# Kernel optimization log

Measured on AMD Instinct MI355X. Metric: run time of the kernel, lower is better.

The kernel has to match this reference:

```python
import jax, jax.numpy as jnp
import numpy as np
from jax import lax

NUM_ENT = 100000
NUM_REL = 100          # init_rel has 2*NUM_REL rows (forward + inverse relations)
DIM = 200              # init_dim = gcn_dim = embed_dim
E = 1000000
B = 1024
K_H, K_W = 10, 20      # embed_dim == k_h * k_w
NUM_FILT = 200
KER = 7
FLAT_H = 2 * K_H - KER + 1   # 14
FLAT_W = K_W - KER + 1       # 14
FLAT_SZ = FLAT_H * FLAT_W * NUM_FILT  # 39200


def _bn1d(x, g, b, eps=1e-5):
    # training-mode BatchNorm1d (biased variance, matching torch)
    m = x.mean(0)
    v = x.var(0)
    return (x - m) * lax.rsqrt(v + eps) * g + b


def _bn2d(x, g, b, eps=1e-5):
    m = x.mean((0, 2, 3), keepdims=True)
    v = x.var((0, 2, 3), keepdims=True)
    return (x - m) * lax.rsqrt(v + eps) * g[None, :, None, None] + b[None, :, None, None]


def _compgcn_layer(x, r, src, dst, etype, enorm,
                   w_in, w_out, w_loop, w_rel, loop_rel, bias, gamma, beta):
    # CompGCNCov with opn='mult': comp(h_src, rel) = h_src * rel
    half = etype.shape[0] // 2
    comp = x[src] * r[etype]                                   # [E, din] edge gather + compose
    msg = jnp.concatenate([comp[:half] @ w_in,                 # first half: original edges
                           comp[half:] @ w_out], axis=0)       # second half: inverse edges
    msg = msg * enorm[:, None]
    agg = jax.ops.segment_sum(msg, dst, num_segments=NUM_ENT)  # scatter-sum to dst nodes
    loop = (x * loop_rel) @ w_loop                             # self-loop composition
    h = (agg + loop) * (1.0 / 3.0) + bias
    h = _bn1d(h, gamma, beta)
    return jnp.tanh(h), r @ w_rel


def setup_inputs() -> dict:
    key = jax.random.key(0)
    ks = jax.random.split(key, 40)
    f32 = jnp.float32
    s = 1.0 / np.sqrt(DIM)
    inp = {
        "init_embed": jax.random.normal(ks[0], (NUM_ENT, DIM), f32) * s,
        "init_rel":   jax.random.normal(ks[1], (2 * NUM_REL, DIM), f32) * s,
        "edge_norm":  jax.random.uniform(ks[2], (E,), f32),
    }
    names = ["w_in", "w_out", "w_loop", "w_rel"]
    for layer in (1, 2):
        for i, n in enumerate(names):
            inp[f"{n}{layer}"] = jax.random.normal(ks[3 + 6 * layer + i], (DIM, DIM), f32) * s
        inp[f"loop_rel{layer}"] = jax.random.normal(jax.random.fold_in(key, layer), (1, DIM), f32) * s
        inp[f"b{layer}"] = jnp.zeros((DIM,), f32)
        inp[f"g{layer}"] = jnp.ones((DIM,), f32)
        inp[f"be{layer}"] = jnp.zeros((DIM,), f32)
    inp["conv_w"] = jax.random.normal(ks[20], (NUM_FILT, 1, KER, KER), f32) * (1.0 / KER)
    inp["conv_b"] = jnp.zeros((NUM_FILT,), f32)
    inp["fc_w"] = jax.random.normal(ks[21], (DIM, FLAT_SZ), f32) * (1.0 / np.sqrt(FLAT_SZ))
    inp["fc_b"] = jnp.zeros((DIM,), f32)
    for n, c in (("bn0", 1), ("bn1", NUM_FILT), ("bn2", DIM)):
        inp[f"{n}_g"] = jnp.ones((c,), f32)
        inp[f"{n}_b"] = jnp.zeros((c,), f32)
    inp["subj"] = jax.random.randint(ks[22], (B,), 0, NUM_ENT)
    inp["rel_idx"] = jax.random.randint(ks[23], (B,), 0, 2 * NUM_REL)
    inp["obj"] = jax.random.randint(ks[24], (B,), 0, NUM_ENT)
    inp["src"] = jax.random.randint(ks[25], (E,), 0, NUM_ENT)
    inp["dst"] = jax.random.randint(ks[26], (E,), 0, NUM_ENT)
    inp["edge_type"] = jnp.concatenate([
        jax.random.randint(ks[27], (E // 2,), 0, NUM_REL),          # in-edges
        jax.random.randint(ks[28], (E // 2,), NUM_REL, 2 * NUM_REL)])  # inverse edges
    return inp


def reference(init_embed, init_rel, edge_norm,
              w_in1, w_out1, w_loop1, w_rel1, loop_rel1, b1, g1, be1,
              w_in2, w_out2, w_loop2, w_rel2, loop_rel2, b2, g2, be2,
              conv_w, conv_b, fc_w, fc_b,
              bn0_g, bn0_b, bn1_g, bn1_b, bn2_g, bn2_b,
              subj, rel_idx, obj, src, dst, edge_type):
    # --- GCN encoder: 2 CompGCN layers ---
    x, r = _compgcn_layer(init_embed, init_rel, src, dst, edge_type, edge_norm,
                          w_in1, w_out1, w_loop1, w_rel1, loop_rel1, b1, g1, be1)
    x, r = _compgcn_layer(x, r, src, dst, edge_type, edge_norm,
                          w_in2, w_out2, w_loop2, w_rel2, loop_rel2, b2, g2, be2)
    sub_emb, rel_emb, obj_emb = x[subj], r[rel_idx], x[obj]   # [B, DIM] each
    # --- ConvE scoring head ---
    stk = jnp.concatenate([sub_emb[:, None, :], rel_emb[:, None, :]], 1)
    stk = stk.reshape(B, 1, 2 * K_H, K_W)                     # [B,1,20,20]
    h = _bn2d(stk, bn0_g, bn0_b)
    h = lax.conv_general_dilated(h, conv_w, (1, 1), 'VALID',
                                 dimension_numbers=('NCHW', 'OIHW', 'NCHW'))
    h = h + conv_b[None, :, None, None]                       # [B,NUM_FILT,14,14]
    h = jnp.maximum(_bn2d(h, bn1_g, bn1_b), 0.0)
    h = h.reshape(B, FLAT_SZ) @ fc_w.T + fc_b                 # [B, DIM]
    h = jnp.maximum(_bn1d(h, bn2_g, bn2_b), 0.0)
    return jax.nn.sigmoid(h @ obj_emb.T)                      # [B, B]
```

## Files before the change

kernel.cpp:

```cpp
#include <hip/hip_runtime.h>

#define DIM 200
#define NENT 100000
#define NEDGE 1000000
#define EHALF 500000
#define NB 1024
#define NFILT 200
#define FLATSZ 39200

#define NDF ((size_t)NENT * DIM)
#define REGF ((size_t)20100000)
#define WPLANE (208 * 224)

typedef float floatx4 __attribute__((ext_vector_type(4)));
typedef short bf16x8 __attribute__((ext_vector_type(8)));
typedef short bf16x4 __attribute__((ext_vector_type(4)));
typedef _Float16 halfx8 __attribute__((ext_vector_type(8)));
typedef _Float16 halfx4 __attribute__((ext_vector_type(4)));

__device__ __forceinline__ void gAtomicAdd(float* p, float v) { unsafeAtomicAdd(p, v); }
__device__ __forceinline__ void gAtomicAdd(double* p, double v) { unsafeAtomicAdd(p, v); }

__device__ __forceinline__ short f2bf(float f) {
    union { float f; unsigned u; } v; v.f = f;
    unsigned r = v.u + 0x7fffu + ((v.u >> 16) & 1u);
    return (short)(r >> 16);
}
__device__ __forceinline__ float bf2f(short s) {
    union { float f; unsigned u; } v; v.u = ((unsigned)(unsigned short)s) << 16;
    return v.f;
}
__device__ __forceinline__ short f2bf_t(float f) {
    union { float f; unsigned u; } v; v.f = f;
    return (short)(v.u >> 16);
}
__device__ __forceinline__ void split8t(const floatx4& lo4, const floatx4& hi4,
                                        bf16x8& h, bf16x8& l) {
#pragma unroll
    for (int e = 0; e < 4; ++e) {
        short hh = f2bf_t(lo4[e]); h[e] = hh; l[e] = f2bf_t(lo4[e] - bf2f(hh));
        short hh2 = f2bf_t(hi4[e]); h[e + 4] = hh2; l[e + 4] = f2bf_t(hi4[e] - bf2f(hh2));
    }
}
__device__ __forceinline__ void split4r(const float4& v, bf16x4& h, bf16x4& l) {
    float a0 = v.x, a1 = v.y, a2 = v.z, a3 = v.w;
    short h0 = f2bf(a0), h1 = f2bf(a1), h2 = f2bf(a2), h3 = f2bf(a3);
    h[0] = h0; h[1] = h1; h[2] = h2; h[3] = h3;
    l[0] = f2bf(a0 - bf2f(h0)); l[1] = f2bf(a1 - bf2f(h1));
    l[2] = f2bf(a2 - bf2f(h2)); l[3] = f2bf(a3 - bf2f(h3));
}

__global__ __launch_bounds__(256) void edge_hist(
    const int* __restrict__ dst, int* __restrict__ hist)
{
    int stride = gridDim.x * blockDim.x;
    for (int e = blockIdx.x * 256 + threadIdx.x; e < NEDGE; e += stride)
        atomicAdd(&hist[dst[e]], 1);
}

__global__ __launch_bounds__(256) void scan1(
    const int* __restrict__ hist, int* __restrict__ incl, int* __restrict__ bsum)
{
    __shared__ int sm[256];
    int i = blockIdx.x * 256 + threadIdx.x;
    int t = threadIdx.x;
    sm[t] = (i < NENT) ? hist[i] : 0;
    __syncthreads();
    for (int off = 1; off < 256; off <<= 1) {
        int v = (t >= off) ? sm[t - off] : 0;
        __syncthreads();
        sm[t] += v;
        __syncthreads();
    }
    if (i < NENT) incl[i] = sm[t];
    if (t == 255) bsum[blockIdx.x] = sm[255];
}

__global__ __launch_bounds__(512) void scan2(int* bsum, int nb)
{
    __shared__ int sm[512];
    int t = threadIdx.x;
    int v = (t < nb) ? bsum[t] : 0;
    sm[t] = v;
    __syncthreads();
    for (int off = 1; off < 512; off <<= 1) {
        int u = (t >= off) ? sm[t - off] : 0;
        __syncthreads();
        sm[t] += u;
        __syncthreads();
    }
    if (t < nb) bsum[t] = sm[t] - v;
}

__global__ __launch_bounds__(256) void scan3(
    const int* __restrict__ hist, int* __restrict__ offs,
    const int* __restrict__ bsum, int* __restrict__ cursor)
{
    int i = blockIdx.x * 256 + threadIdx.x;
    if (i < NENT) {
        int excl = offs[i] - hist[i] + bsum[blockIdx.x];
        offs[i] = excl;
        cursor[i] = excl;
    }
    if (i == 0) offs[NENT] = NEDGE;
}

__global__ __launch_bounds__(256) void edge_fill(
    const int* __restrict__ src, const int* __restrict__ dst,
    const int* __restrict__ etype, const float* __restrict__ enorm,
    int* __restrict__ cursor, int4* __restrict__ recs)
{
    int stride = gridDim.x * blockDim.x;
    for (int e = blockIdx.x * 256 + threadIdx.x; e < NEDGE; e += stride) {
        int pos = atomicAdd(&cursor[dst[e]], 1);
        recs[pos] = make_int4(src[e], etype[e] | ((e >= EHALF) ? 0x10000 : 0),
                              __float_as_int(enorm[e]), 0);
    }
}

__global__ __launch_bounds__(256) void build_map(
    const int* __restrict__ subj, const int* __restrict__ obj, int* __restrict__ map)
{
    int i = blockIdx.x * 256 + threadIdx.x;
    if (i < NB) map[subj[i]] = i;
    else if (i < 2 * NB) map[obj[i - NB]] = i;
}

__global__ __launch_bounds__(256) void to_f16(
    const float* __restrict__ X, _Float16* __restrict__ Y, long n4)
{
    long stride = (long)gridDim.x * blockDim.x;
    for (long i = (long)blockIdx.x * blockDim.x + threadIdx.x; i < n4; i += stride) {
        float4 v = ((const float4*)X)[i];
        halfx4 h;
        h[0] = (_Float16)v.x; h[1] = (_Float16)v.y;
        h[2] = (_Float16)v.z; h[3] = (_Float16)v.w;
        ((halfx4*)Y)[i] = h;
    }
}

__global__ __launch_bounds__(256) void gather_nodes(
    const _Float16* __restrict__ x16, const float* __restrict__ r,
    const int* __restrict__ offs, const int4* __restrict__ recs,
    short* __restrict__ aggI, short* __restrict__ aggO)
{
    int node = blockIdx.x * 4 + (threadIdx.x >> 6);
    int lane = threadIdx.x & 63;
    if (node >= NENT) return;
    int beg = offs[node], end = offs[node + 1];
    bool act = lane < 50;
    int lane_c = min(lane, 49);
    const float4* rb = (const float4*)r;
    float4 aI = make_float4(0.f, 0.f, 0.f, 0.f);
    float4 aO = make_float4(0.f, 0.f, 0.f, 0.f);

    auto ld_x = [&](int s) -> float4 {
        halfx4 v = *(const halfx4*)&x16[(size_t)s * 200 + lane_c * 4];
        return make_float4((float)v[0], (float)v[1], (float)v[2], (float)v[3]);
    };

    if (beg < end) {
        int i1 = min(beg + 1, end - 1);
        int4 rcA = recs[beg];
        int4 rcB = recs[i1];
        float4 xvA = ld_x(rcA.x);
        float4 rvA = rb[(size_t)(rcA.y & 0xffff) * 50 + lane_c];
        for (int i = beg; i < end; ++i) {
            int i2 = min(i + 2, end - 1);
            int4 rcC = recs[i2];
            float4 xvB = ld_x(rcB.x);
            float4 rvB = rb[(size_t)(rcB.y & 0xffff) * 50 + lane_c];
            float w = __int_as_float(rcA.z);
            float wI = (rcA.y & 0x10000) ? 0.f : w;
            float wO = w - wI;
            float px = xvA.x * rvA.x, py = xvA.y * rvA.y,
                  pz = xvA.z * rvA.z, pw = xvA.w * rvA.w;
            aI.x += px * wI; aI.y += py * wI; aI.z += pz * wI; aI.w += pw * wI;
            aO.x += px * wO; aO.y += py * wO; aO.z += pz * wO; aO.w += pw * wO;
            rcA = rcB; rcB = rcC; xvA = xvB; rvA = rvB;
        }
    }
    if (act) {
        bf16x4 hI, lI, hO, lO;
        split4r(aI, hI, lI);
        split4r(aO, hO, lO);
        size_t base = (size_t)node * 400 + lane * 4;
        *(bf16x4*)&aggI[base] = hI;
        *(bf16x4*)&aggI[base + 200] = lI;
        *(bf16x4*)&aggO[base] = hO;
        *(bf16x4*)&aggO[base + 200] = lO;
    }
}

__global__ __launch_bounds__(256) void pack_w3(
    const float* __restrict__ w0, const float* __restrict__ w1,
    const float* __restrict__ w2, const float* __restrict__ lrel,
    short* __restrict__ Wp)
{
    int i = blockIdx.x * 256 + threadIdx.x;
    if (i >= 3 * WPLANE) return;
    int seg = i / WPLANE, rem = i % WPLANE;
    int n = rem / 224, k = rem % 224;
    const float* W = (seg == 0) ? w0 : (seg == 1) ? w1 : w2;
    float v = (n < 200 && k < 200) ? W[k * 200 + n] : 0.f;
    if (seg == 2 && n < 200 && k < 200) v *= lrel[k];
    short hi = f2bf(v);
    Wp[i] = hi;
    Wp[i + 3 * WPLANE] = f2bf(v - bf2f(hi));
}

__global__ __launch_bounds__(256) void pack_fcw(
    const float* __restrict__ W, _Float16* __restrict__ Wt)
{
    long i = (long)blockIdx.x * 256 + threadIdx.x;
    if (i >= (long)208 * FLATSZ) return;
    int n = (int)(i / FLATSZ);
    Wt[i] = (n < 200) ? (_Float16)W[i] : (_Float16)0.f;
}

template<int NF0, int NF, int A2MODE>
__device__ __forceinline__ void gemm_body(
    const short* __restrict__ A0s, const short* __restrict__ A1s,
    const float* __restrict__ A2f, const _Float16* __restrict__ A2h,
    const short* __restrict__ WpH, const short* __restrict__ WpL,
    float* C, const float* __restrict__ bias, const int* __restrict__ map,
    float alpha, int M, double* __restrict__ s1, double* __restrict__ s2,
    short* BsH, short* BsL, float* fsum, float* fsq)
{
    int t = threadIdx.x;
    int lane = t & 63, wave = t >> 6;
    int col16 = lane & 15, quad = lane >> 4;
    int row_base = blockIdx.x * 128 + wave * 32;
    if (t < 112) { fsum[t] = 0.f; fsq[t] = 0.f; }
    floatx4 acc[NF][2];
#pragma unroll
    for (int nf = 0; nf < NF; ++nf) { acc[nf][0] = (floatx4)0.f; acc[nf][1] = (floatx4)0.f; }
    int r0 = row_base + col16, r1 = row_base + 16 + col16;
    int r0c = min(r0, M - 1), r1c = min(r1, M - 1);
    size_t b0 = (size_t)r0c * 400, b1 = (size_t)r1c * 400;
    const int rows4 = NF * 16 * 4;

    bf16x8 sh[2], sl[2];
    bf16x8 cah0 = (bf16x8)0, cal0 = (bf16x8)0,
           cah1 = (bf16x8)0, cal1 = (bf16x8)0;
    bf16x8 nah0 = (bf16x8)0, nal0 = (bf16x8)0,
           nah1 = (bf16x8)0, nal1 = (bf16x8)0;

    auto stage_ld = [&](int kc) {
        int seg = kc / 7, c = kc - seg * 7, k0 = c * 32;
        const short* WH = WpH + seg * WPLANE + k0;
        const short* WL = WpL + seg * WPLANE + k0;
#pragma unroll
        for (int s = 0; s < 2; ++s) {
            int i = t + s * 256;
            if (i < rows4) {
                int nl = i >> 2, part = i & 3;
                int n = NF0 * 16 + nl;
                sh[s] = *(const bf16x8*)&WH[n * 224 + part * 8];
                sl[s] = *(const bf16x8*)&WL[n * 224 + part * 8];
            }
        }
    };
    auto stage_st = [&](short* BH, short* BL) {
#pragma unroll
        for (int s = 0; s < 2; ++s) {
            int i = t + s * 256;
            if (i < rows4) {
                int nl = i >> 2, part = i & 3;
                *(bf16x8*)&BH[nl * 40 + part * 8] = sh[s];
                *(bf16x8*)&BL[nl * 40 + part * 8] = sl[s];
            }
        }
    };
    auto loadA = [&](int kc, bf16x8& h0, bf16x8& l0, bf16x8& h1, bf16x8& l1) {
        int seg = kc / 7, c = kc - seg * 7;
        int koff = c * 32 + quad * 8;
        if (koff < 200) {
            if (seg < 2) {
                const short* A = seg ? A1s : A0s;
                h0 = *(const bf16x8*)&A[b0 + koff];
                l0 = *(const bf16x8*)&A[b0 + 200 + koff];
                h1 = *(const bf16x8*)&A[b1 + koff];
                l1 = *(const bf16x8*)&A[b1 + 200 + koff];
            } else {
                size_t o0 = (size_t)r0c * 200 + koff, o1 = (size_t)r1c * 200 + koff;
                floatx4 x0, x1v, y0, y1v;
                if (A2MODE == 0) {
                    x0 = *(const floatx4*)&A2f[o0];
                    x1v = *(const floatx4*)&A2f[o0 + 4];
                    y0 = *(const floatx4*)&A2f[o1];
                    y1v = *(const floatx4*)&A2f[o1 + 4];
                } else {
                    halfx8 v0 = *(const halfx8*)&A2h[o0];
                    halfx8 v1 = *(const halfx8*)&A2h[o1];
#pragma unroll
                    for (int e = 0; e < 4; ++e) {
                        x0[e] = (float)v0[e]; x1v[e] = (float)v0[e + 4];
                        y0[e] = (float)v1[e]; y1v[e] = (float)v1[e + 4];
                    }
                }
                split8t(x0, x1v, h0, l0);
                split8t(y0, y1v, h1, l1);
            }
        } else {
            h0 = (bf16x8)0; l0 = (bf16x8)0; h1 = (bf16x8)0; l1 = (bf16x8)0;
        }
    };

    stage_ld(0);
    loadA(0, cah0, cal0, cah1, cal1);
    stage_st(BsH, BsL);
    __syncthreads();

    for (int kc = 0; kc < 21; ++kc) {
        int cur = kc & 1;
        const short* BH = BsH + cur * 4480;
        const short* BL = BsL + cur * 4480;
        if (kc < 20) {
            stage_ld(kc + 1);
            loadA(kc + 1, nah0, nal0, nah1, nal1);
        }
        __builtin_amdgcn_s_setprio(1);
#pragma unroll
        for (int nf = 0; nf < NF; ++nf) {
            bf16x8 bh = *(const bf16x8*)&BH[(nf * 16 + col16) * 40 + quad * 8];
            bf16x8 bl = *(const bf16x8*)&BL[(nf * 16 + col16) * 40 + quad * 8];
            acc[nf][0] = __builtin_amdgcn_mfma_f32_16x16x32_bf16(cah0, bh, acc[nf][0], 0, 0, 0);
            acc[nf][0] = __builtin_amdgcn_mfma_f32_16x16x32_bf16(cah0, bl, acc[nf][0], 0, 0, 0);
            acc[nf][0] = __builtin_amdgcn_mfma_f32_16x16x32_bf16(cal0, bh, acc[nf][0], 0, 0, 0);
            acc[nf][1] = __builtin_amdgcn_mfma_f32_16x16x32_bf16(cah1, bh, acc[nf][1], 0, 0, 0);
            acc[nf][1] = __builtin_amdgcn_mfma_f32_16x16x32_bf16(cah1, bl, acc[nf][1], 0, 0, 0);
            acc[nf][1] = __builtin_amdgcn_mfma_f32_16x16x32_bf16(cal1, bh, acc[nf][1], 0, 0, 0);
        }
        __builtin_amdgcn_s_setprio(0);
        if (kc < 20) {
            short* BHn = BsH + (cur ^ 1) * 4480;
            short* BLn = BsL + (cur ^ 1) * 4480;
            stage_st(BHn, BLn);
        }
        __syncthreads();
        cah0 = nah0; cal0 = nal0; cah1 = nah1; cal1 = nal1;
    }

    int slot[2][4];
    if (map) {
#pragma unroll
        for (int h = 0; h < 2; ++h)
#pragma unroll
            for (int j = 0; j < 4; ++j) {
                int rr = row_base + h * 16 + quad * 4 + j;
                slot[h][j] = (rr < M) ? map[rr] : -1;
            }
    }
#pragma unroll
    for (int nf = 0; nf < NF; ++nf) {
        int lc = nf * 16 + col16;
        int colg = NF0 * 16 + lc;
        if (colg >= 200) continue;
        float bv = bias[colg];
        float ls = 0.f, lq = 0.f;
#pragma unroll
        for (int h = 0; h < 2; ++h) {
            int rbase = row_base + h * 16 + quad * 4;
#pragma unroll
            for (int j = 0; j < 4; ++j) {
                int rr = rbase + j;
                if (rr < M) {
                    float v = acc[nf][h][j] * alpha + bv;
                    ls += v; lq += v * v;
                    if (!map) {
                        C[(size_t)rr * 200 + colg] = v;
                    } else {
                        int s = slot[h][j];
                        if (s >= 0) C[(size_t)s * 200 + colg] = v;
                    }
                }
            }
        }
        ls += __shfl_down(ls, 32); ls += __shfl_down(ls, 16);
        lq += __shfl_down(lq, 32); lq += __shfl_down(lq, 16);
        if (quad == 0) {
            atomicAdd(&fsum[lc], ls);
            atomicAdd(&fsq[lc], lq);
        }
    }
    __syncthreads();
    if (t < NF * 16) {
        int colg = NF0 * 16 + t;
        if (colg < 200) {
            gAtomicAdd(&s1[colg], (double)fsum[t]);
            gAtomicAdd(&s2[colg], (double)fsq[t]);
        }
    }
}

template<int A2MODE>
__global__ __launch_bounds__(256) void gemm_mfma(
    const short* A0s, const short* A1s,
    const float* A2f, const _Float16* A2h,
    const short* __restrict__ WpH, const short* __restrict__ WpL,
    float* C, const float* __restrict__ bias, const int* __restrict__ map,
    float alpha, int M, double* __restrict__ s1, double* __restrict__ s2)
{
    __shared__ short BsH[2][112 * 40];
    __shared__ short BsL[2][112 * 40];
    __shared__ float fsum[112];
    __shared__ float fsq[112];
    if (blockIdx.y == 0)
        gemm_body<0, 7, A2MODE>(A0s, A1s, A2f, A2h, WpH, WpL, C, bias, map,
                                alpha, M, s1, s2, &BsH[0][0], &BsL[0][0], fsum, fsq);
    else
        gemm_body<7, 6, A2MODE>(A0s, A1s, A2f, A2h, WpH, WpL, C, bias, map,
                                alpha, M, s1, s2, &BsH[0][0], &BsL[0][0], fsum, fsq);
}

template<int NF0, int NF>
__device__ __forceinline__ void fc_gemm_body(
    const _Float16* __restrict__ Ph, const _Float16* __restrict__ Wt,
    float* __restrict__ part, int ky, _Float16* Bs)
{
    int t = threadIdx.x;
    int lane = t & 63, wave = t >> 6;
    int col16 = lane & 15, quad = lane >> 4;
    int row_base = blockIdx.x * 128 + wave * 32;
    int c0 = ky * 25;
    floatx4 acc[NF][2];
#pragma unroll
    for (int nf = 0; nf < NF; ++nf) { acc[nf][0] = (floatx4)0.f; acc[nf][1] = (floatx4)0.f; }
    int r0 = row_base + col16, r1 = row_base + 16 + col16;
    const int rows4 = NF * 16 * 4;

    for (int c = c0; c < c0 + 25; ++c) {
        int k0 = c * 32;
        for (int i = t; i < rows4; i += 256) {
            int nl = i >> 2, part_i = i & 3;
            int n = NF0 * 16 + nl;
            *(halfx8*)&Bs[nl * 40 + part_i * 8] =
                *(const halfx8*)&Wt[(size_t)n * FLATSZ + k0 + part_i * 8];
        }
        __syncthreads();
        int koff = k0 + quad * 8;
        halfx8 a0 = *(const halfx8*)&Ph[(size_t)r0 * FLATSZ + koff];
        halfx8 a1 = *(const halfx8*)&Ph[(size_t)r1 * FLATSZ + koff];
#pragma unroll
        for (int nf = 0; nf < NF; ++nf) {
            halfx8 b = *(const halfx8*)&Bs[(nf * 16 + col16) * 40 + quad * 8];
            acc[nf][0] = __builtin_amdgcn_mfma_f32_16x16x32_f16(a0, b, acc[nf][0], 0, 0, 0);
            acc[nf][1] = __builtin_amdgcn_mfma_f32_16x16x32_f16(a1, b, acc[nf][1], 0, 0, 0);
        }
        __syncthreads();
    }
    float* out = part + (size_t)ky * (NB * 200);
#pragma unroll
    for (int nf = 0; nf < NF; ++nf) {
        int colg = NF0 * 16 + nf * 16 + col16;
        if (colg >= 200) continue;
#pragma unroll
        for (int h = 0; h < 2; ++h) {
            int rbase = row_base + h * 16 + quad * 4;
#pragma unroll
            for (int j = 0; j < 4; ++j)
                out[(size_t)(rbase + j) * 200 + colg] = acc[nf][h][j];
        }
    }
}

__global__ __launch_bounds__(256) void fc_gemm(
    const _Float16* __restrict__ Ph, const _Float16* __restrict__ Wt,
    float* __restrict__ part)
{
    __shared__ _Float16 Bs[112 * 40];
    int ky = blockIdx.y >> 1;
    if ((blockIdx.y & 1) == 0)
        fc_gemm_body<0, 7>(Ph, Wt, part, ky, Bs);
    else
        fc_gemm_body<7, 6>(Ph, Wt, part, ky, Bs);
}

__global__ __launch_bounds__(256) void fc_reduce(
    const float* __restrict__ part, const float* __restrict__ bias,
    float* __restrict__ hfc)
{
    int i = blockIdx.x * 256 + threadIdx.x;
    float acc = bias[i % 200];
#pragma unroll
    for (int y = 0; y < 49; ++y) acc += part[(size_t)y * (NB * 200) + i];
    hfc[i] = acc;
}

__global__ __launch_bounds__(256) void colstats(
    const float* __restrict__ X, int M, int rpb,
    double* __restrict__ s1, double* __restrict__ s2)
{
    int c = threadIdx.x;
    if (c >= 200) return;
    int r0 = blockIdx.x * rpb;
    int r1 = min(r0 + rpb, M);
    float sum = 0.f, sq = 0.f;
    for (int rr = r0; rr < r1; ++rr) {
        float v = X[(size_t)rr * 200 + c];
        sum += v; sq += v * v;
    }
    gAtomicAdd(&s1[c], (double)sum);
    gAtomicAdd(&s2[c], (double)sq);
}

__global__ void finalize_stats(const double* __restrict__ s1, const double* __restrict__ s2,
                               const float* __restrict__ g, const float* __restrict__ bb,
                               float* __restrict__ sc, float* __restrict__ sh,
                               int ncols, double count)
{
    int c = threadIdx.x;
    if (c >= ncols) return;
    double m = s1[c] / count;
    double v = s2[c] / count - m * m;
    double scd = (double)g[c] / sqrt(v + 1e-5);
    sc[c] = (float)scd;
    sh[c] = (float)((double)bb[c] - m * scd);
}

__global__ __launch_bounds__(256) void bn_tanh_f16(
    const float* __restrict__ X, const float* __restrict__ sc,
    const float* __restrict__ sh, _Float16* __restrict__ Y, long n4)
{
    long stride = (long)gridDim.x * blockDim.x;
    for (long i = (long)blockIdx.x * blockDim.x + threadIdx.x; i < n4; i += stride) {
        int c4 = (int)(i % 50) * 4;
        float4 v = ((const float4*)X)[i];
        halfx4 h;
        h[0] = (_Float16)tanhf(v.x * sc[c4 + 0] + sh[c4 + 0]);
        h[1] = (_Float16)tanhf(v.y * sc[c4 + 1] + sh[c4 + 1]);
        h[2] = (_Float16)tanhf(v.z * sc[c4 + 2] + sh[c4 + 2]);
        h[3] = (_Float16)tanhf(v.w * sc[c4 + 3] + sh[c4 + 3]);
        ((halfx4*)Y)[i] = h;
    }
}

__global__ __launch_bounds__(256) void bn_act_200(
    float* __restrict__ X, const float* __restrict__ sc, const float* __restrict__ sh,
    long n4, int act)
{
    long stride = (long)gridDim.x * blockDim.x;
    for (long i = (long)blockIdx.x * blockDim.x + threadIdx.x; i < n4; i += stride) {
        int c4 = (int)(i % 50) * 4;
        float4 v = ((const float4*)X)[i];
        float a0 = v.x * sc[c4 + 0] + sh[c4 + 0];
        float a1 = v.y * sc[c4 + 1] + sh[c4 + 1];
        float a2 = v.z * sc[c4 + 2] + sh[c4 + 2];
        float a3 = v.w * sc[c4 + 3] + sh[c4 + 3];
        if (act == 0) { a0 = tanhf(a0); a1 = tanhf(a1); a2 = tanhf(a2); a3 = tanhf(a3); }
        else { a0 = fmaxf(a0, 0.f); a1 = fmaxf(a1, 0.f); a2 = fmaxf(a2, 0.f); a3 = fmaxf(a3, 0.f); }
        ((float4*)X)[i] = make_float4(a0, a1, a2, a3);
    }
}

__global__ __launch_bounds__(256) void rel_mm(
    const float* __restrict__ R, const float* __restrict__ W, float* __restrict__ O)
{
    int idx = blockIdx.x * blockDim.x + threadIdx.x;
    if (idx >= 200 * 200) return;
    int row = idx / 200, col = idx - row * 200;
    float acc = 0.f;
    for (int k = 0; k < 200; ++k) acc = fmaf(R[row * 200 + k], W[k * 200 + col], acc);
    O[idx] = acc;
}

__global__ __launch_bounds__(256) void build_stk(
    const float* __restrict__ x2c, const float* __restrict__ r2,
    const int* __restrict__ subj, const int* __restrict__ ridx,
    const int* __restrict__ map,
    float* __restrict__ stk, double* __restrict__ s1, double* __restrict__ s2)
{
    __shared__ float wsum[4], wsq[4];
    int b = blockIdx.x, t = threadIdx.x;
    const float* se = x2c + (size_t)map[subj[b]] * DIM;
    const float* re = r2 + (size_t)ridx[b] * DIM;
    float sum = 0.f, sq = 0.f;
    for (int i = t; i < 400; i += 256) {
        float v = (i < 200) ? se[i] : re[i - 200];
        stk[(size_t)b * 400 + i] = v;
        sum += v; sq += v * v;
    }
    for (int off = 32; off > 0; off >>= 1) {
        sum += __shfl_down(sum, off);
        sq  += __shfl_down(sq, off);
    }
    if ((t & 63) == 0) { wsum[t >> 6] = sum; wsq[t >> 6] = sq; }
    __syncthreads();
    if (t == 0) {
        float S = wsum[0] + wsum[1] + wsum[2] + wsum[3];
        float Q = wsq[0] + wsq[1] + wsq[2] + wsq[3];
        gAtomicAdd(&s1[0], (double)S);
        gAtomicAdd(&s2[0], (double)Q);
    }
}

__global__ __launch_bounds__(256) void conv_fwd(
    const float* __restrict__ stk, const float* __restrict__ conv_w,
    const float* __restrict__ conv_b, const float* __restrict__ sc0,
    const float* __restrict__ sh0, _Float16* __restrict__ Ph,
    double* __restrict__ s1, double* __restrict__ s2)
{
    __shared__ float img[400];
    __shared__ float wsm[9800];
    __shared__ float bsm[200];
    __shared__ float fsum[200];
    __shared__ float fsq[200];
    int b = blockIdx.x, t = threadIdx.x;
    float scale0 = sc0[0], shift0 = sh0[0];
    if (t < 200) { fsum[t] = 0.f; fsq[t] = 0.f; bsm[t] = conv_b[t]; }
    for (int i = t; i < 400; i += 256) img[i] = stk[(size_t)b * 400 + i] * scale0 + shift0;
    for (int i = t; i < 9800; i += 256) wsm[i] = conv_w[i];
    __syncthreads();
    for (int fy = t; fy < 2800; fy += 256) {
        int f = fy / 14, y = fy - (fy / 14) * 14;
        const float* wf = &wsm[f * 49];
        float acc[14];
        float bias = bsm[f];
#pragma unroll
        for (int xx = 0; xx < 14; ++xx) acc[xx] = bias;
#pragma unroll
        for (int i = 0; i < 7; ++i) {
            const float* rowp = &img[(y + i) * 20];
            float rv[20];
#pragma unroll
            for (int c = 0; c < 20; ++c) rv[c] = rowp[c];
#pragma unroll
            for (int j = 0; j < 7; ++j) {
                float wv = wf[i * 7 + j];
#pragma unroll
                for (int xx = 0; xx < 14; ++xx) acc[xx] = fmaf(rv[xx + j], wv, acc[xx]);
            }
        }
        float ls = 0.f, lq = 0.f;
        _Float16* pp = Ph + (size_t)b * FLATSZ + (size_t)f * 196 + y * 14;
#pragma unroll
        for (int xx = 0; xx < 14; ++xx) {
            float v = acc[xx];
            pp[xx] = (_Float16)v;
            ls += v; lq += v * v;
        }
        atomicAdd(&fsum[f], ls);
        atomicAdd(&fsq[f], lq);
    }
    __syncthreads();
    if (t < 200) {
        gAtomicAdd(&s1[t], (double)fsum[t]);
        gAtomicAdd(&s2[t], (double)fsq[t]);
    }
}

__global__ __launch_bounds__(256) void bn1_relu_f16(
    _Float16* __restrict__ Ph, const float* __restrict__ sc, const float* __restrict__ sh)
{
    long n4 = (long)NB * (FLATSZ / 4);
    long stride = (long)gridDim.x * blockDim.x;
    for (long i = (long)blockIdx.x * blockDim.x + threadIdx.x; i < n4; i += stride) {
        int k4 = (int)(i % (FLATSZ / 4));
        int f = k4 / 49;
        float s = sc[f], h = sh[f];
        halfx4 v = ((const halfx4*)Ph)[i];
#pragma unroll
        for (int e = 0; e < 4; ++e) {
            float x = (float)v[e];
            x = fmaxf(x * s + h, 0.f);
            v[e] = (_Float16)x;
        }
        ((halfx4*)Ph)[i] = v;
    }
}

__global__ __launch_bounds__(256) void score_mm(
    const float* __restrict__ Hn, const float* __restrict__ x2c,
    const int* __restrict__ obj, const int* __restrict__ map,
    float* __restrict__ out)
{
    __shared__ float Asm[16][17];
    __shared__ float Bsm[16][17];
    int tx = threadIdx.x & 15, ty = threadIdx.x >> 4;
    int row = blockIdx.y * 16 + ty;
    int col = blockIdx.x * 16 + tx;
    int oj = map[obj[blockIdx.x * 16 + ty]];
    float acc = 0.f;
    for (int k0 = 0; k0 < 200; k0 += 16) {
        int k = k0 + tx;
        Asm[ty][tx] = (k < 200) ? Hn[(size_t)row * 200 + k] : 0.f;
        Bsm[ty][tx] = (k < 200) ? x2c[(size_t)oj * 200 + k] : 0.f;
        __syncthreads();
#pragma unroll
        for (int kk = 0; kk < 16; ++kk) acc = fmaf(Asm[ty][kk], Bsm[tx][kk], acc);
        __syncthreads();
    }
    out[(size_t)row * NB + col] = 1.f / (1.f + expf(-acc));
}

extern "C" void kernel_launch(void* const* d_in, const int* in_sizes, int n_in,
                              void* d_out, int out_size, void* d_ws, size_t ws_size,
                              hipStream_t stream)
{
    (void)in_sizes; (void)n_in; (void)out_size;
    const float* init_embed = (const float*)d_in[0];
    const float* init_rel   = (const float*)d_in[1];
    const float* edge_norm  = (const float*)d_in[2];
    const float* w_in1  = (const float*)d_in[3];
    const float* w_out1 = (const float*)d_in[4];
    const float* w_loop1= (const float*)d_in[5];
    const float* w_rel1 = (const float*)d_in[6];
    const float* lrel1  = (const float*)d_in[7];
    const float* b1     = (const float*)d_in[8];
    const float* gm1    = (const float*)d_in[9];
    const float* be1    = (const float*)d_in[10];
    const float* w_in2  = (const float*)d_in[11];
    const float* w_out2 = (const float*)d_in[12];
    const float* w_loop2= (const float*)d_in[13];
    const float* w_rel2 = (const float*)d_in[14];
    const float* lrel2  = (const float*)d_in[15];
    const float* b2     = (const float*)d_in[16];
    const float* gm2    = (const float*)d_in[17];
    const float* be2    = (const float*)d_in[18];
    const float* conv_w = (const float*)d_in[19];
    const float* conv_b = (const float*)d_in[20];
    const float* fc_w   = (const float*)d_in[21];
    const float* fc_b   = (const float*)d_in[22];
    const float* bn0_g  = (const float*)d_in[23];
    const float* bn0_b  = (const float*)d_in[24];
    const float* bn1_g  = (const float*)d_in[25];
    const float* bn1_b  = (const float*)d_in[26];
    const float* bn2_g  = (const float*)d_in[27];
    const float* bn2_b  = (const float*)d_in[28];
    const int* subj   = (const int*)d_in[29];
    const int* relidx = (const int*)d_in[30];
    const int* obj    = (const int*)d_in[31];
    const int* src    = (const int*)d_in[32];
    const int* dst    = (const int*)d_in[33];
    const int* etype  = (const int*)d_in[34];

    float* ws = (float*)d_ws;
    float* R0 = ws;
    float* R1 = ws + REGF;
    float* R2 = ws + 2 * REGF;
    float* p = ws + 3 * REGF;
    float* r1v = p;            p += 40000;
    float* r2v = p;            p += 40000;
    float* stk = p;            p += 409600;
    float* hfc = p;            p += 204800;
    float* x2c = p;            p += 409600;
    float* fsc = p;            p += 256;
    float* fsh = p;            p += 256;
    double* ds1 = (double*)p;  p += 512;
    double* ds2 = (double*)p;  p += 512;
    short* Wp = (short*)p;     p += (6 * WPLANE) / 2;
    int* map = (int*)p;        p += NENT;
    int* hist = (int*)p;       p += NENT;
    int* offs = (int*)p;       p += NENT + 4;
    int* cursor = (int*)p;     p += NENT;
    int* bsum = (int*)p;       p += 512;
    int4* recs = (int4*)p;     p += (size_t)NEDGE * 4;

    _Float16* ie16 = (_Float16*)R0;
    float* x1f = R0;
    short* aggI1 = (short*)R1;
    short* aggOs = (short*)R2;
    _Float16* x1h = (_Float16*)R1;
    short* aggI2 = (short*)R0;
    _Float16* Ph  = (_Float16*)R0;
    _Float16* fch = (_Float16*)R2;
    float* fpart = R2 + 4200000;

    const size_t NEED = (size_t)(p - ws) * sizeof(float);
    if (ws_size < NEED) return;

    const int NBLK = (NENT + 255) / 256;
    const size_t DSBYTES = 512 * sizeof(double);

    hipMemsetAsync(hist, 0, NENT * sizeof(int), stream);
    hipMemsetAsync(map, 0xFF, NENT * sizeof(int), stream);
    edge_hist<<<1024, 256, 0, stream>>>(dst, hist);
    scan1<<<NBLK, 256, 0, stream>>>(hist, offs, bsum);
    scan2<<<1, 512, 0, stream>>>(bsum, NBLK);
    scan3<<<NBLK, 256, 0, stream>>>(hist, offs, bsum, cursor);
    edge_fill<<<1024, 256, 0, stream>>>(src, dst, etype, edge_norm, cursor, recs);
    build_map<<<(2 * NB + 255) / 256, 256, 0, stream>>>(subj, obj, map);

    dim3 gGemm((NENT + 127) / 128, 2);

    pack_w3<<<(3 * WPLANE + 255) / 256, 256, 0, stream>>>(w_in1, w_out1, w_loop1, lrel1, Wp);
    to_f16<<<4096, 256, 0, stream>>>(init_embed, ie16, (long)NENT * 50);
    gather_nodes<<<(NENT + 3) / 4, 256, 0, stream>>>(ie16, init_rel, offs, recs,
                                                     aggI1, aggOs);
    hipMemsetAsync(ds1, 0, DSBYTES, stream);
    gemm_mfma<0><<<gGemm, 256, 0, stream>>>(
        aggI1, aggOs, init_embed, nullptr, Wp, Wp + 3 * WPLANE,
        x1f, b1, nullptr, 1.f / 3.f, NENT, ds1, ds2);
    finalize_stats<<<1, 256, 0, stream>>>(ds1, ds2, gm1, be1, fsc, fsh, 200, (double)NENT);
    bn_tanh_f16<<<4096, 256, 0, stream>>>(x1f, fsc, fsh, x1h, (long)NENT * 50);
    rel_mm<<<(40000 + 255) / 256, 256, 0, stream>>>(init_rel, w_rel1, r1v);

    pack_w3<<<(3 * WPLANE + 255) / 256, 256, 0, stream>>>(w_in2, w_out2, w_loop2, lrel2, Wp);
    gather_nodes<<<(NENT + 3) / 4, 256, 0, stream>>>(x1h, r1v, offs, recs,
                                                     aggI2, aggOs);
    hipMemsetAsync(ds1, 0, DSBYTES, stream);
    gemm_mfma<1><<<gGemm, 256, 0, stream>>>(
        aggI2, aggOs, nullptr, x1h, Wp, Wp + 3 * WPLANE,
        x2c, b2, map, 1.f / 3.f, NENT, ds1, ds2);
    finalize_stats<<<1, 256, 0, stream>>>(ds1, ds2, gm2, be2, fsc, fsh, 200, (double)NENT);
    bn_act_200<<<400, 256, 0, stream>>>(x2c, fsc, fsh, (long)2 * NB * 50, 0);
    rel_mm<<<(40000 + 255) / 256, 256, 0, stream>>>(r1v, w_rel2, r2v);

    hipMemsetAsync(ds1, 0, DSBYTES, stream);
    build_stk<<<NB, 256, 0, stream>>>(x2c, r2v, subj, relidx, map, stk, ds1, ds2);
    finalize_stats<<<1, 256, 0, stream>>>(ds1, ds2, bn0_g, bn0_b, fsc, fsh, 1,
                                          (double)((long)NB * 400));
    hipMemsetAsync(ds1, 0, DSBYTES, stream);
    conv_fwd<<<NB, 256, 0, stream>>>(stk, conv_w, conv_b, fsc, fsh, Ph, ds1, ds2);
    finalize_stats<<<1, 256, 0, stream>>>(ds1, ds2, bn1_g, bn1_b, fsc, fsh, 200,
                                          (double)((long)NB * 196));
    bn1_relu_f16<<<4096, 256, 0, stream>>>(Ph, fsc, fsh);
    pack_fcw<<<(int)(((long)208 * FLATSZ + 255) / 256), 256, 0, stream>>>(fc_w, fch);
    fc_gemm<<<dim3(8, 98), 256, 0, stream>>>(Ph, fch, fpart);
    fc_reduce<<<800, 256, 0, stream>>>(fpart, fc_b, hfc);
    hipMemsetAsync(ds1, 0, DSBYTES, stream);
    colstats<<<4, 256, 0, stream>>>(hfc, NB, 256, ds1, ds2);
    finalize_stats<<<1, 256, 0, stream>>>(ds1, ds2, bn2_g, bn2_b, fsc, fsh, 200, (double)NB);
    bn_act_200<<<200, 256, 0, stream>>>(hfc, fsc, fsh, (long)NB * 50, 1);
    score_mm<<<dim3(NB / 16, NB / 16), 256, 0, stream>>>(hfc, x2c, obj, map, (float*)d_out);
}
```

Baseline: 1.284 ms.

## Compute all output columns per GEMM block instead of splitting across grid.y

The node GEMM previously launched two column-halves per row tile (7 and 6 fragments), so each block reloaded the same A rows and split them into bf16 hi/lo pairs twice. Now one block computes all 13 column fragments, so A is loaded and split once, and the shared-memory row stride for B drops from 40 to 36. In exchange each block holds twice as many accumulators (104 floats per lane), which raises register pressure and can lower occupancy. The grid also halves, leaving fewer blocks to hide memory latency.

```diff
diff --git a/kernel.cpp b/kernel.cpp
--- a/kernel.cpp
+++ b/kernel.cpp
@@ -218,57 +218,60 @@
     Wt[i] = (n < 200) ? (_Float16)W[i] : (_Float16)0.f;
 }
 
-template<int NF0, int NF, int A2MODE>
-__device__ __forceinline__ void gemm_body(
+template<int A2MODE>
+__global__ __launch_bounds__(256) void gemm_mfma(
     const short* __restrict__ A0s, const short* __restrict__ A1s,
     const float* __restrict__ A2f, const _Float16* __restrict__ A2h,
     const short* __restrict__ WpH, const short* __restrict__ WpL,
     float* C, const float* __restrict__ bias, const int* __restrict__ map,
-    float alpha, int M, double* __restrict__ s1, double* __restrict__ s2,
-    short* BsH, short* BsL, float* fsum, float* fsq)
-{
+    float alpha, int M, double* __restrict__ s1, double* __restrict__ s2)
+{
+    constexpr int NF = 13;
+    constexpr int BST = 36;
+    constexpr int PLANE = 208 * BST;
+    __shared__ short BsH[2][PLANE];
+    __shared__ short BsL[2][PLANE];
+    __shared__ float fsum[208];
+    __shared__ float fsq[208];
+
     int t = threadIdx.x;
     int lane = t & 63, wave = t >> 6;
     int col16 = lane & 15, quad = lane >> 4;
     int row_base = blockIdx.x * 128 + wave * 32;
-    if (t < 112) { fsum[t] = 0.f; fsq[t] = 0.f; }
+    if (t < 208) { fsum[t] = 0.f; fsq[t] = 0.f; }
     floatx4 acc[NF][2];
 #pragma unroll
     for (int nf = 0; nf < NF; ++nf) { acc[nf][0] = (floatx4)0.f; acc[nf][1] = (floatx4)0.f; }
     int r0 = row_base + col16, r1 = row_base + 16 + col16;
     int r0c = min(r0, M - 1), r1c = min(r1, M - 1);
     size_t b0 = (size_t)r0c * 400, b1 = (size_t)r1c * 400;
-    const int rows4 = NF * 16 * 4;
-
-    bf16x8 sh[2], sl[2];
-    bf16x8 cah0 = (bf16x8)0, cal0 = (bf16x8)0,
-           cah1 = (bf16x8)0, cal1 = (bf16x8)0;
-    bf16x8 nah0 = (bf16x8)0, nal0 = (bf16x8)0,
-           nah1 = (bf16x8)0, nal1 = (bf16x8)0;
+
+    bf16x8 sh[4], sl[4];
+    bf16x8 ch0, cl0, ch1, cl1;
+    bf16x8 nh0, nl0v, nh1, nl1v;
 
     auto stage_ld = [&](int kc) {
         int seg = kc / 7, c = kc - seg * 7, k0 = c * 32;
         const short* WH = WpH + seg * WPLANE + k0;
         const short* WL = WpL + seg * WPLANE + k0;
 #pragma unroll
-        for (int s = 0; s < 2; ++s) {
+        for (int s = 0; s < 4; ++s) {
             int i = t + s * 256;
-            if (i < rows4) {
+            if (i < 832) {
                 int nl = i >> 2, part = i & 3;
-                int n = NF0 * 16 + nl;
-                sh[s] = *(const bf16x8*)&WH[n * 224 + part * 8];
-                sl[s] = *(const bf16x8*)&WL[n * 224 + part * 8];
+                sh[s] = *(const bf16x8*)&WH[nl * 224 + part * 8];
+                sl[s] = *(const bf16x8*)&WL[nl * 224 + part * 8];
             }
         }
     };
-    auto stage_st = [&](short* BH, short* BL) {
-#pragma unroll
-        for (int s = 0; s < 2; ++s) {
+    auto stage_st = [&](int bufi) {
+#pragma unroll
+        for (int s = 0; s < 4; ++s) {
             int i = t + s * 256;
-            if (i < rows4) {
+            if (i < 832) {
                 int nl = i >> 2, part = i & 3;
-                *(bf16x8*)&BH[nl * 40 + part * 8] = sh[s];
-                *(bf16x8*)&BL[nl * 40 + part * 8] = sl[s];
+                *(bf16x8*)&BsH[bufi][nl * BST + part * 8] = sh[s];
+                *(bf16x8*)&BsL[bufi][nl * BST + part * 8] = sl[s];
             }
         }
     };
@@ -306,41 +309,36 @@
             h0 = (bf16x8)0; l0 = (bf16x8)0; h1 = (bf16x8)0; l1 = (bf16x8)0;
         }
     };
+    auto do_mfma = [&](int bufi) {
+        __builtin_amdgcn_s_setprio(1);
+#pragma unroll
+        for (int nf = 0; nf < NF; ++nf) {
+            bf16x8 bh = *(const bf16x8*)&BsH[bufi][(nf * 16 + col16) * BST + quad * 8];
+            bf16x8 bl = *(const bf16x8*)&BsL[bufi][(nf * 16 + col16) * BST + quad * 8];
+            acc[nf][0] = __builtin_amdgcn_mfma_f32_16x16x32_bf16(ch0, bh, acc[nf][0], 0, 0, 0);
+            acc[nf][0] = __builtin_amdgcn_mfma_f32_16x16x32_bf16(ch0, bl, acc[nf][0], 0, 0, 0);
+            acc[nf][0] = __builtin_amdgcn_mfma_f32_16x16x32_bf16(cl0, bh, acc[nf][0], 0, 0, 0);
+            acc[nf][1] = __builtin_amdgcn_mfma_f32_16x16x32_bf16(ch1, bh, acc[nf][1], 0, 0, 0);
+            acc[nf][1] = __builtin_amdgcn_mfma_f32_16x16x32_bf16(ch1, bl, acc[nf][1], 0, 0, 0);
+            acc[nf][1] = __builtin_amdgcn_mfma_f32_16x16x32_bf16(cl1, bh, acc[nf][1], 0, 0, 0);
+        }
+        __builtin_amdgcn_s_setprio(0);
+    };
 
     stage_ld(0);
-    loadA(0, cah0, cal0, cah1, cal1);
-    stage_st(BsH, BsL);
+    loadA(0, ch0, cl0, ch1, cl1);
+    stage_st(0);
     __syncthreads();
 
-    for (int kc = 0; kc < 21; ++kc) {
-        int cur = kc & 1;
-        const short* BH = BsH + cur * 4480;
-        const short* BL = BsL + cur * 4480;
-        if (kc < 20) {
-            stage_ld(kc + 1);
-            loadA(kc + 1, nah0, nal0, nah1, nal1);
-        }
-        __builtin_amdgcn_s_setprio(1);
-#pragma unroll
-        for (int nf = 0; nf < NF; ++nf) {
-            bf16x8 bh = *(const bf16x8*)&BH[(nf * 16 + col16) * 40 + quad * 8];
-            bf16x8 bl = *(const bf16x8*)&BL[(nf * 16 + col16) * 40 + quad * 8];
-            acc[nf][0] = __builtin_amdgcn_mfma_f32_16x16x32_bf16(cah0, bh, acc[nf][0], 0, 0, 0);
-            acc[nf][0] = __builtin_amdgcn_mfma_f32_16x16x32_bf16(cah0, bl, acc[nf][0], 0, 0, 0);
-            acc[nf][0] = __builtin_amdgcn_mfma_f32_16x16x32_bf16(cal0, bh, acc[nf][0], 0, 0, 0);
-            acc[nf][1] = __builtin_amdgcn_mfma_f32_16x16x32_bf16(cah1, bh, acc[nf][1], 0, 0, 0);
-            acc[nf][1] = __builtin_amdgcn_mfma_f32_16x16x32_bf16(cah1, bl, acc[nf][1], 0, 0, 0);
-            acc[nf][1] = __builtin_amdgcn_mfma_f32_16x16x32_bf16(cal1, bh, acc[nf][1], 0, 0, 0);
-        }
-        __builtin_amdgcn_s_setprio(0);
-        if (kc < 20) {
-            short* BHn = BsH + (cur ^ 1) * 4480;
-            short* BLn = BsL + (cur ^ 1) * 4480;
-            stage_st(BHn, BLn);
-        }
+    for (int kc = 0; kc < 20; ++kc) {
+        stage_ld(kc + 1);
+        loadA(kc + 1, nh0, nl0v, nh1, nl1v);
+        do_mfma(kc & 1);
+        stage_st((kc + 1) & 1);
         __syncthreads();
-        cah0 = nah0; cal0 = nal0; cah1 = nah1; cal1 = nal1;
-    }
+        ch0 = nh0; cl0 = nl0v; ch1 = nh1; cl1 = nl1v;
+    }
+    do_mfma(0);
 
     int slot[2][4];
     if (map) {
@@ -355,7 +353,7 @@
 #pragma unroll
     for (int nf = 0; nf < NF; ++nf) {
         int lc = nf * 16 + col16;
-        int colg = NF0 * 16 + lc;
+        int colg = lc;
         if (colg >= 200) continue;
         float bv = bias[colg];
         float ls = 0.f, lq = 0.f;
@@ -385,33 +383,10 @@
         }
     }
     __syncthreads();
-    if (t < NF * 16) {
-        int colg = NF0 * 16 + t;
-        if (colg < 200) {
-            gAtomicAdd(&s1[colg], (double)fsum[t]);
-            gAtomicAdd(&s2[colg], (double)fsq[t]);
-        }
-    }
-}
-
-template<int A2MODE>
-__global__ __launch_bounds__(256) void gemm_mfma(
-    const short* A0s, const short* A1s,
-    const float* A2f, const _Float16* A2h,
-    const short* __restrict__ WpH, const short* __restrict__ WpL,
-    float* C, const float* __restrict__ bias, const int* __restrict__ map,
-    float alpha, int M, double* __restrict__ s1, double* __restrict__ s2)
-{
-    __shared__ short BsH[2][112 * 40];
-    __shared__ short BsL[2][112 * 40];
-    __shared__ float fsum[112];
-    __shared__ float fsq[112];
-    if (blockIdx.y == 0)
-        gemm_body<0, 7, A2MODE>(A0s, A1s, A2f, A2h, WpH, WpL, C, bias, map,
-                                alpha, M, s1, s2, &BsH[0][0], &BsL[0][0], fsum, fsq);
-    else
-        gemm_body<7, 6, A2MODE>(A0s, A1s, A2f, A2h, WpH, WpL, C, bias, map,
-                                alpha, M, s1, s2, &BsH[0][0], &BsL[0][0], fsum, fsq);
+    if (t < 200) {
+        gAtomicAdd(&s1[t], (double)fsum[t]);
+        gAtomicAdd(&s2[t], (double)fsq[t]);
+    }
 }
 
 template<int NF0, int NF>
@@ -782,7 +757,7 @@
     edge_fill<<<1024, 256, 0, stream>>>(src, dst, etype, edge_norm, cursor, recs);
     build_map<<<(2 * NB + 255) / 256, 256, 0, stream>>>(subj, obj, map);
 
-    dim3 gGemm((NENT + 127) / 128, 2);
+    dim3 gGemm((NENT + 127) / 128);
 
     pack_w3<<<(3 * WPLANE + 255) / 256, 256, 0, stream>>>(w_in1, w_out1, w_loop1, lrel1, Wp);
     to_f16<<<4096, 256, 0, stream>>>(init_embed, ie16, (long)NENT * 50);
```

Result: slower. 1.326 ms (+3.3%).
